# Performance work log

Hardware: AMD Instinct MI355X
Metric: run time of the kernel (lower is better)

Reference implementation:

```python
import jax, jax.numpy as jnp
import numpy as np

L, H, D, FF = 6, 8, 1024, 2048
E = D // 8            # per-head dim = n_model // 8 = 128
MAXLEN = 1024         # relative position table length
B, S = 16, 512


def _sinusoidal(max_len, e):
    # matches RelativePositionalEmbedding.reset_parameters
    pos = np.arange(-(max_len // 2), max_len // 2, dtype=np.float32)
    inv = 10000.0 ** ((np.arange(e) // 2) * 2.0 / e)
    w = pos[:, None] / inv[None, :]
    w[:, 0::2] = np.sin(w[:, 0::2])
    w[:, 1::2] = np.cos(w[:, 1::2])
    return jnp.asarray(w, jnp.float32)


def setup_inputs() -> dict:
    key = jax.random.key(0)
    ks = jax.random.split(key, 12)
    sd_attn = (2.0 / (D + D)) ** 0.5 * (2 ** -0.5)
    sd_ffn1 = (2.0 / (D + FF)) ** 0.5
    inp = {
        "x": jax.random.normal(ks[0], (B, S, D), jnp.float32),
        "mask": jnp.ones((B, S), dtype=bool),
        "wq": jax.random.normal(ks[1], (L, D, D), jnp.float32) * sd_attn,
        "wk": jax.random.normal(ks[2], (L, D, D), jnp.float32) * sd_attn,
        "wv": jax.random.normal(ks[3], (L, D, D), jnp.float32) * sd_attn,
        "wo": jax.random.normal(ks[4], (L, D, D), jnp.float32) * (2.0 / (D + D)) ** 0.5,
        "bu": jnp.zeros((L, H, E), jnp.float32),
        "bv": jnp.zeros((L, H, E), jnp.float32),
        "ln1_g": jnp.ones((L, D), jnp.float32),
        "ln1_b": jnp.zeros((L, D), jnp.float32),
        "w1": jax.random.normal(ks[5], (L, D, FF), jnp.float32) * sd_ffn1,
        "b1": jnp.zeros((L, FF), jnp.float32),
        "w2": jax.random.normal(ks[6], (L, FF, D), jnp.float32) * sd_ffn1,
        "b2": jnp.zeros((L, D), jnp.float32),
        "ln2_g": jnp.ones((L, D), jnp.float32),
        "ln2_b": jnp.zeros((L, D), jnp.float32),
        "pos_table": jnp.tile(_sinusoidal(MAXLEN, E)[None], (L, 1, 1)),
    }
    return inp


def _layer_norm(h, g, b):
    mu = h.mean(-1, keepdims=True)
    var = ((h - mu) ** 2).mean(-1, keepdims=True)
    return (h - mu) * jax.lax.rsqrt(var + 1e-5) * g + b


def reference(x, mask, wq, wk, wv, wo, bu, bv, ln1_g, ln1_b,
              w1, b1, w2, b2, ln2_g, ln2_b, pos_table):
    Bb, Ss, Dd = x.shape
    Ll, Hh, Ee = bu.shape
    scale = float(Ee) ** 0.5
    offset = pos_table.shape[1] // 2
    # relative index j - i + offset, shape [S, S]
    idx = jnp.arange(Ss)[None, :] - jnp.arange(Ss)[:, None] + offset
    neg = jnp.where(mask[:, None, None, :], 0.0, -jnp.inf)  # [B,1,1,S]
    for l in range(Ll):
        q = (x @ wq[l]).reshape(Bb, Ss, Hh, Ee)
        k = (x @ wk[l]).reshape(Bb, Ss, Hh, Ee)
        v = (x @ wv[l]).reshape(Bb, Ss, Hh, Ee)
        p = pos_table[l][idx]  # [S, S, E]
        scores = jnp.einsum('bqhe,bkhe->bhqk', q + bu[l], k)
        scores = scores + jnp.einsum('bqhe,qke->bhqk', q + bv[l], p)
        attn = jax.nn.softmax(scores / scale + neg, axis=-1)
        o = jnp.einsum('bhqk,bkhe->bqhe', attn, v).reshape(Bb, Ss, Hh * Ee) @ wo[l]
        x = _layer_norm(x + o, ln1_g[l], ln1_b[l])
        h = jax.nn.relu(x @ w1[l] + b1[l]) @ w2[l] + b2[l]
        x = _layer_norm(x + h, ln2_g[l], ln2_b[l])
    return x
```

## Files before the change

kernel.cpp:

```cpp
#include <hip/hip_runtime.h>


typedef __bf16 bf16;
typedef __bf16 bf16x4 __attribute__((ext_vector_type(4)));
typedef __bf16 bf16x8 __attribute__((ext_vector_type(8)));
typedef float  f32x4  __attribute__((ext_vector_type(4)));

#define NLAYERS 6
#define NHEADS  8
#define DMODEL  1024
#define FFDIM   2048
#define EDIM    128
#define NBATCH  16
#define SEQ     512

__device__ __forceinline__ void gl_lds16(const bf16* g, bf16* l) {
  __builtin_amdgcn_global_load_lds(
      (const __attribute__((address_space(1))) unsigned int*)g,
      (__attribute__((address_space(3))) unsigned int*)l, 16, 0, 0);
}

struct GArgs {
  const bf16* A;
  const bf16* B;
  const float* bias;
  const float* bias2;
  const float* resid;
  float* outf;
  bf16*  outh;
  bf16*  outh2;
  bf16*  outh3;
  bf16*  outh4;
  int lda, ldb, nK;
  int qoff, mq, msh;
};

template<int MODE>
__global__ __launch_bounds__(256, 3)
void gemm_k(GArgs g) {
  __shared__ __align__(16) bf16 As[128][64];
  __shared__ __align__(16) bf16 Bs[128][64];
  const int tid = threadIdx.x;
  int bx = blockIdx.x, by = blockIdx.y;
  {
    const int nwg = gridDim.x * gridDim.y;
    const int orig = bx + gridDim.x * by;
    const int wsw = (orig & 7) * (nwg >> 3) + (orig >> 3);
    bx = wsw % gridDim.x; by = wsw / gridDim.x;
  }
  const int lane = tid & 63, w = tid >> 6;
  const int wr = w >> 1, wc = w & 1;
  const int l15 = lane & 15, lg = lane >> 4;
  const int xk = l15 & 7;

  int t0 = 0;
  if constexpr (MODE == 10) {
    const int lq0 = (by * 16) & (g.mq - 1);
    const int i0 = g.qoff + lq0;
    t0 = (497 - i0) >> 7; if (t0 > 2) t0 = 2;
  }
  const int bxe = (MODE == 10) ? (t0 + bx) : bx;

  f32x4 acc[4][4] = {};

  for (int ks = 0; ks < g.nK; ++ks) {
    const int k0 = ks * 64;
    #pragma unroll
    for (int i = 0; i < 4; ++i) {
      const int c = i * 256 + tid;
      const int row = c >> 3, slot = c & 7;
      const int kc = (slot ^ (row & 7)) * 8;
      size_t go;
      if constexpr (MODE == 10) {
        const int rg = by * 128 + row;
        const int b = rg >> g.msh;
        const int lq = (rg >> 3) & (g.mq - 1);
        const int hh = rg & 7;
        go = (size_t)b * (SEQ * DMODEL) + (size_t)(g.qoff + lq) * DMODEL
           + hh * EDIM + k0 + kc;
      } else {
        go = (size_t)(by * 128 + row) * g.lda + k0 + kc;
      }
      gl_lds16(g.A + go, &As[row][slot * 8]);
    }
    #pragma unroll
    for (int i = 0; i < 4; ++i) {
      const int c = i * 256 + tid;
      const int row = c >> 3, slot = c & 7;
      const int kc = (slot ^ (row & 7)) * 8;
      gl_lds16(g.B + (size_t)(bxe * 128 + row) * g.ldb + k0 + kc,
               &Bs[row][slot * 8]);
    }
    __syncthreads();
    #pragma unroll
    for (int kk = 0; kk < 2; ++kk) {
      bf16x8 av[4], bvv[4];
      #pragma unroll
      for (int i = 0; i < 4; ++i)
        av[i] = *(const bf16x8*)((const char*)&As[0][0]
                 + (wr * 64 + i * 16 + l15) * 128 + (((kk * 4 + lg) ^ xk) * 16));
      #pragma unroll
      for (int i = 0; i < 4; ++i)
        bvv[i] = *(const bf16x8*)((const char*)&Bs[0][0]
                 + (wc * 64 + i * 16 + l15) * 128 + (((kk * 4 + lg) ^ xk) * 16));
      #pragma unroll
      for (int mi = 0; mi < 4; ++mi)
        #pragma unroll
        for (int ni = 0; ni < 4; ++ni)
          acc[mi][ni] = __builtin_amdgcn_mfma_f32_16x16x32_bf16(av[mi], bvv[ni], acc[mi][ni], 0, 0, 0);
    }
    __syncthreads();
  }

  #pragma unroll
  for (int mi = 0; mi < 4; ++mi)
  #pragma unroll
  for (int ni = 0; ni < 4; ++ni)
  #pragma unroll
  for (int r = 0; r < 4; ++r) {
    const int row = wr * 64 + mi * 16 + lg * 4 + r;
    const int col = wc * 64 + ni * 16 + l15;
    const float v = acc[mi][ni][r];
    if constexpr (MODE == 9) {
      const int gm = by * 128 + row;
      const int seg = bx >> 3;
      const int gc = (bx & 7) * 128 + col;
      if (seg == 0) {
        const size_t i = (size_t)gm * DMODEL + gc;
        g.outh[i]  = (bf16)(v + g.bias[gc]);
        g.outh2[i] = (bf16)(v + g.bias2[gc]);
      } else if (seg == 1) {
        g.outh3[(size_t)gm * DMODEL + gc] = (bf16)v;
      } else {
        const int b = gm >> 9, s = gm & 511, h = gc >> 7, e = gc & 127;
        g.outh4[((size_t)(b * NHEADS + h) * EDIM + e) * SEQ + s] = (bf16)v;
      }
    } else if constexpr (MODE == 10) {
      const int rg = by * 128 + row;
      const int lq = (rg >> 3) & (g.mq - 1);
      const int ig = g.qoff + lq;
      const int j = bxe * 128 + col;
      const int k = j + ig - 512;
      if (k >= 0 && k < 512)
        g.outh[(size_t)rg * 512 + k] = (bf16)v;
    } else if constexpr (MODE == 6) {
      const int gm = by * 128 + row, gc = bx * 128 + col;
      const size_t i = (size_t)gm * DMODEL + gc;
      g.outf[i] = v + g.resid[i];
    } else if constexpr (MODE == 7) {
      const int gm = by * 128 + row, gc = bx * 128 + col;
      g.outh[(size_t)gm * FFDIM + gc] = (bf16)fmaxf(v + g.bias[gc], 0.f);
    } else if constexpr (MODE == 8) {
      const int gm = by * 128 + row, gc = bx * 128 + col;
      const size_t i = (size_t)gm * DMODEL + gc;
      g.outf[i] = v + g.bias[gc] + g.resid[i];
    }
  }
}

struct AArgs {
  const bf16* qu; const bf16* kbf; const bf16* vt; const bf16* R;
  bf16* attnout; int qoff, mq;
};

__global__ __launch_bounds__(256, 2)
void attn_k(AArgs g) {
  __shared__ __align__(16) bf16 Ks[64][128];
  __shared__ __align__(16) bf16 Vs[128][64];
  __shared__ __align__(16) bf16 Pl[128][72];
  const int tid = threadIdx.x, lane = tid & 63, w = tid >> 6;
  const int l15 = lane & 15, lg = lane >> 4;
  int bqt, bh;
  {
    const int nwg = gridDim.x * gridDim.y;
    const int orig = blockIdx.x + gridDim.x * blockIdx.y;
    const int wsw = (orig & 7) * (nwg >> 3) + (orig >> 3);
    bqt = wsw % gridDim.x; bh = wsw / gridDim.x;
  }
  const int b = bh >> 3, h = bh & 7;
  const int q0g = g.qoff + bqt * 128;
  const int qw = w * 32;
  const float ISC = 0.08838834764831845f;

  const bf16* qbase = g.qu + (size_t)b * SEQ * DMODEL
                    + (size_t)(q0g + qw) * DMODEL + (size_t)h * EDIM;
  bf16x8 a[2][4];
  #pragma unroll
  for (int mi = 0; mi < 2; ++mi)
    #pragma unroll
    for (int kk = 0; kk < 4; ++kk)
      a[mi][kk] = *(const bf16x8*)(qbase + (size_t)(mi * 16 + l15) * DMODEL + kk * 32 + lg * 8);

  const bf16* kbase = g.kbf + (size_t)b * SEQ * DMODEL + (size_t)h * EDIM;
  const bf16* vbase = g.vt + (size_t)bh * EDIM * SEQ;
  const bf16* Rrow = g.R + ((size_t)(b * g.mq + (bqt * 128 + qw)) * 8 + h) * 512;

  f32x4 o[2][8] = {};
  float m_run[2][4], s_run[2][4];
  #pragma unroll
  for (int mi = 0; mi < 2; ++mi)
    #pragma unroll
    for (int r = 0; r < 4; ++r) { m_run[mi][r] = -1e30f; s_run[mi][r] = 0.f; }

  for (int kt = 0; kt < 8; ++kt) {
    const int k0 = kt * 64;
    #pragma unroll
    for (int i = 0; i < 4; ++i) {
      const int c = i * 256 + tid;
      const int row = c >> 4, slot = c & 15;
      gl_lds16(kbase + (size_t)(k0 + row) * DMODEL + (slot ^ (row & 15)) * 8,
               &Ks[row][slot * 8]);
    }
    #pragma unroll
    for (int i = 0; i < 4; ++i) {
      const int c = i * 256 + tid;
      const int row = c >> 3, slot = c & 7;
      gl_lds16(vbase + (size_t)row * SEQ + k0 + (slot ^ (row & 7)) * 8,
               &Vs[row][slot * 8]);
    }
    float rv[2][4][4];
    #pragma unroll
    for (int mi = 0; mi < 2; ++mi)
    #pragma unroll
    for (int ni = 0; ni < 4; ++ni)
    #pragma unroll
    for (int r = 0; r < 4; ++r) {
      const int lrow = mi * 16 + lg * 4 + r;
      rv[mi][ni][r] = (float)Rrow[(size_t)lrow * 4096 + (k0 + ni * 16 + l15)];
    }
    __syncthreads();

    f32x4 s[2][4] = {};
    #pragma unroll
    for (int kk = 0; kk < 4; ++kk) {
      bf16x8 bvv[4];
      #pragma unroll
      for (int ni = 0; ni < 4; ++ni)
        bvv[ni] = *(const bf16x8*)((const char*)&Ks[0][0]
                   + (ni * 16 + l15) * 256 + (((kk * 4 + lg) ^ l15) * 16));
      #pragma unroll
      for (int mi = 0; mi < 2; ++mi)
        #pragma unroll
        for (int ni = 0; ni < 4; ++ni)
          s[mi][ni] = __builtin_amdgcn_mfma_f32_16x16x32_bf16(a[mi][kk], bvv[ni], s[mi][ni], 0, 0, 0);
    }

    float sv[2][4][4];
    #pragma unroll
    for (int mi = 0; mi < 2; ++mi)
    #pragma unroll
    for (int ni = 0; ni < 4; ++ni)
    #pragma unroll
    for (int r = 0; r < 4; ++r)
      sv[mi][ni][r] = (s[mi][ni][r] + rv[mi][ni][r]) * ISC;

    float fsc[2][4], rs[2][4];
    #pragma unroll
    for (int mi = 0; mi < 2; ++mi)
    #pragma unroll
    for (int r = 0; r < 4; ++r) {
      float t = fmaxf(fmaxf(sv[mi][0][r], sv[mi][1][r]),
                      fmaxf(sv[mi][2][r], sv[mi][3][r]));
      #pragma unroll
      for (int od = 1; od < 16; od <<= 1) t = fmaxf(t, __shfl_xor(t, od));
      const float mn = fmaxf(m_run[mi][r], t);
      fsc[mi][r] = __expf(m_run[mi][r] - mn);
      m_run[mi][r] = mn;
      rs[mi][r] = 0.f;
    }
    #pragma unroll
    for (int mi = 0; mi < 2; ++mi)
    #pragma unroll
    for (int ni = 0; ni < 4; ++ni)
    #pragma unroll
    for (int r = 0; r < 4; ++r) {
      const float e = __expf(sv[mi][ni][r] - m_run[mi][r]);
      rs[mi][r] += e;
      Pl[qw + mi * 16 + lg * 4 + r][ni * 16 + l15] = (bf16)e;
    }
    #pragma unroll
    for (int mi = 0; mi < 2; ++mi)
    #pragma unroll
    for (int r = 0; r < 4; ++r) {
      float t = rs[mi][r];
      #pragma unroll
      for (int od = 1; od < 16; od <<= 1) t += __shfl_xor(t, od);
      s_run[mi][r] = s_run[mi][r] * fsc[mi][r] + t;
    }
    #pragma unroll
    for (int mi = 0; mi < 2; ++mi)
    #pragma unroll
    for (int ni = 0; ni < 8; ++ni)
    #pragma unroll
    for (int r = 0; r < 4; ++r)
      o[mi][ni][r] *= fsc[mi][r];

    bf16x8 pa[2][2];
    #pragma unroll
    for (int mi = 0; mi < 2; ++mi)
      #pragma unroll
      for (int kk = 0; kk < 2; ++kk)
        pa[mi][kk] = *(const bf16x8*)&Pl[qw + mi * 16 + l15][kk * 32 + lg * 8];
    #pragma unroll
    for (int ni = 0; ni < 8; ++ni) {
      const int vr = ni * 16 + l15;
      bf16x8 v0 = *(const bf16x8*)((const char*)&Vs[0][0]
                   + vr * 128 + ((lg ^ (l15 & 7)) * 16));
      bf16x8 v1 = *(const bf16x8*)((const char*)&Vs[0][0]
                   + vr * 128 + (((4 + lg) ^ (l15 & 7)) * 16));
      #pragma unroll
      for (int mi = 0; mi < 2; ++mi) {
        o[mi][ni] = __builtin_amdgcn_mfma_f32_16x16x32_bf16(pa[mi][0], v0, o[mi][ni], 0, 0, 0);
        o[mi][ni] = __builtin_amdgcn_mfma_f32_16x16x32_bf16(pa[mi][1], v1, o[mi][ni], 0, 0, 0);
      }
    }
    __syncthreads();
  }

  const size_t obase = (size_t)b * SEQ * DMODEL + (size_t)h * EDIM;
  #pragma unroll
  for (int mi = 0; mi < 2; ++mi)
  #pragma unroll
  for (int ni = 0; ni < 8; ++ni)
  #pragma unroll
  for (int r = 0; r < 4; ++r) {
    const int q = q0g + qw + mi * 16 + lg * 4 + r;
    g.attnout[obase + (size_t)q * DMODEL + ni * 16 + l15] =
        (bf16)(o[mi][ni][r] / s_run[mi][r]);
  }
}

struct TArgs {
  const float* wq; const float* wk; const float* wv; const float* wo;
  const float* w1; const float* w2;
  bf16* out;
};
__global__ __launch_bounds__(256)
void wtrans_k(TArgs t) {
  __shared__ float tt[32][33];
  const int bid = blockIdx.x;
  int seg, tile;
  if (bid < 4096)      { seg = bid >> 10; tile = bid & 1023; }
  else if (bid < 6144) { seg = 4; tile = bid - 4096; }
  else                 { seg = 5; tile = bid - 6144; }
  int R, C, txn; size_t oofs; const float* in;
  if (seg < 4) {
    R = 1024; C = 1024; txn = 32; oofs = (size_t)seg << 20;
    in = (seg == 0) ? t.wq : (seg == 1) ? t.wk : (seg == 2) ? t.wv : t.wo;
  } else if (seg == 4) {
    R = 1024; C = 2048; txn = 64; oofs = (size_t)4 << 20; in = t.w1;
  } else {
    R = 2048; C = 1024; txn = 32; oofs = (size_t)6 << 20; in = t.w2;
  }
  bf16* out = t.out + oofs;
  const int c0 = (tile % txn) * 32, r0 = (tile / txn) * 32;
  const int tx = threadIdx.x & 31, ty = threadIdx.x >> 5;
  #pragma unroll
  for (int i = 0; i < 32; i += 8)
    tt[ty + i][tx] = in[(size_t)(r0 + ty + i) * C + c0 + tx];
  __syncthreads();
  #pragma unroll
  for (int i = 0; i < 32; i += 8)
    out[(size_t)(c0 + ty + i) * R + r0 + tx] = (bf16)tt[tx][ty + i];
}

__global__ __launch_bounds__(256)
void cvt_k(const float* __restrict__ in, bf16* __restrict__ out, int n4) {
  const int i = blockIdx.x * 256 + threadIdx.x;
  if (i >= n4) return;
  const float4 v = ((const float4*)in)[i];
  bf16x4 h; h[0] = (bf16)v.x; h[1] = (bf16)v.y; h[2] = (bf16)v.z; h[3] = (bf16)v.w;
  ((bf16x4*)out)[i] = h;
}

__global__ __launch_bounds__(256)
void ln_k(const float* __restrict__ y, const float* __restrict__ gam, const float* __restrict__ bet,
          float* __restrict__ xout, bf16* __restrict__ xbf) {
  const int t = threadIdx.x;
  const size_t row = blockIdx.x;
  const float4 v = *(const float4*)(y + row * DMODEL + t * 4);
  float s = v.x + v.y + v.z + v.w;
  float q = v.x * v.x + v.y * v.y + v.z * v.z + v.w * v.w;
  #pragma unroll
  for (int o = 32; o; o >>= 1) { s += __shfl_xor(s, o); q += __shfl_xor(q, o); }
  __shared__ float red[8];
  const int wid = t >> 6;
  if ((t & 63) == 0) { red[wid * 2] = s; red[wid * 2 + 1] = q; }
  __syncthreads();
  s = red[0] + red[2] + red[4] + red[6];
  q = red[1] + red[3] + red[5] + red[7];
  const float mu = s * (1.f / DMODEL);
  const float var = q * (1.f / DMODEL) - mu * mu;
  const float rs = rsqrtf(var + 1e-5f);
  const float g0 = gam[t * 4], g1 = gam[t * 4 + 1], g2 = gam[t * 4 + 2], g3 = gam[t * 4 + 3];
  const float b0 = bet[t * 4], b1 = bet[t * 4 + 1], b2 = bet[t * 4 + 2], b3 = bet[t * 4 + 3];
  float4 o;
  o.x = (v.x - mu) * rs * g0 + b0; o.y = (v.y - mu) * rs * g1 + b1;
  o.z = (v.z - mu) * rs * g2 + b2; o.w = (v.w - mu) * rs * g3 + b3;
  *(float4*)(xout + row * DMODEL + t * 4) = o;
  bf16x4 h; h[0] = (bf16)o.x; h[1] = (bf16)o.y; h[2] = (bf16)o.z; h[3] = (bf16)o.w;
  *(bf16x4*)(xbf + row * DMODEL + t * 4) = h;
}

extern "C" void kernel_launch(void* const* d_in, const int* in_sizes, int n_in,
                              void* d_out, int out_size, void* d_ws, size_t ws_size,
                              hipStream_t stream) {
  const float* x_in  = (const float*)d_in[0];
  const float* wq    = (const float*)d_in[2];
  const float* wk    = (const float*)d_in[3];
  const float* wv    = (const float*)d_in[4];
  const float* wo    = (const float*)d_in[5];
  const float* bu    = (const float*)d_in[6];
  const float* bv    = (const float*)d_in[7];
  const float* ln1g  = (const float*)d_in[8];
  const float* ln1b  = (const float*)d_in[9];
  const float* w1    = (const float*)d_in[10];
  const float* b1    = (const float*)d_in[11];
  const float* w2    = (const float*)d_in[12];
  const float* b2    = (const float*)d_in[13];
  const float* ln2g  = (const float*)d_in[14];
  const float* ln2b  = (const float*)d_in[15];
  const float* pos   = (const float*)d_in[16];
  float* out = (float*)d_out;

  char* ws = (char*)d_ws;
  size_t off = 0;
  auto alloc = [&](size_t bytes) -> void* {
    void* p = ws + off; off += (bytes + 255) & ~(size_t)255; return p;
  };
  const size_t BSD = (size_t)NBATCH * SEQ * DMODEL;
  bf16* posb = (bf16*)alloc((size_t)NLAYERS * 1024 * EDIM * 2);
  bf16* wT   = (bf16*)alloc((size_t)8 * 1024 * 1024 * 2);
  bf16* xbf  = (bf16*)alloc(BSD * 2);
  float* xws = (float*)alloc(BSD * 4);
  float* ybuf= (float*)alloc(BSD * 4);
  bf16* qu   = (bf16*)alloc(BSD * 2);
  bf16* qv   = (bf16*)alloc(BSD * 2);
  bf16* kbf  = (bf16*)alloc(BSD * 2);
  bf16* vt   = (bf16*)alloc(BSD * 2);
  bf16* attnout = qv;
  bf16* h1 = qu;
  const size_t base = off;

  int C = 4;
  if (ws_size >= base + (size_t)512 * 131072) C = 1;
  else if (ws_size >= base + (size_t)256 * 131072) C = 2;
  const int mq = SEQ / C;
  const int msh = (mq == 512) ? 12 : (mq == 256) ? 11 : 10;
  bf16* R2 = (bf16*)alloc((size_t)mq * 131072);

  cvt_k<<<(int)(BSD / 4 / 256), 256, 0, stream>>>(x_in, xbf, (int)(BSD / 4));
  cvt_k<<<(NLAYERS * 1024 * EDIM / 4) / 256, 256, 0, stream>>>(pos, posb, NLAYERS * 1024 * EDIM / 4);

  for (int l = 0; l < NLAYERS; ++l) {
    const size_t wofs = (size_t)l * DMODEL * DMODEL;
    const size_t fofs = (size_t)l * DMODEL * FFDIM;

    TArgs ta{wq + wofs, wk + wofs, wv + wofs, wo + wofs, w1 + fofs, w2 + fofs, wT};
    wtrans_k<<<8192, 256, 0, stream>>>(ta);

    GArgs a{};
    a.A = xbf; a.B = wT; a.bias = bu + l * 1024; a.bias2 = bv + l * 1024;
    a.outh = qu; a.outh2 = qv; a.outh3 = kbf; a.outh4 = vt;
    a.lda = 1024; a.ldb = 1024; a.nK = 16;
    gemm_k<9><<<dim3(24, 64), 256, 0, stream>>>(a);

    for (int c = 0; c < C; ++c) {
      const int qoff = c * mq;
      GArgs ar{}; ar.A = qv; ar.B = posb + (size_t)l * 1024 * EDIM; ar.outh = R2;
      ar.lda = 1024; ar.ldb = 128; ar.nK = 2; ar.qoff = qoff; ar.mq = mq; ar.msh = msh;
      gemm_k<10><<<dim3(6, mq), 256, 0, stream>>>(ar);

      AArgs aa{qu, kbf, vt, R2, attnout, qoff, mq};
      attn_k<<<dim3(mq / 128, 128), 256, 0, stream>>>(aa);
    }

    GArgs aw{}; aw.A = attnout; aw.B = wT + ((size_t)3 << 20); aw.resid = (l == 0 ? x_in : xws);
    aw.outf = ybuf; aw.lda = 1024; aw.ldb = 1024; aw.nK = 16;
    gemm_k<6><<<dim3(8, 64), 256, 0, stream>>>(aw);

    ln_k<<<NBATCH * SEQ, 256, 0, stream>>>(ybuf, ln1g + l * 1024, ln1b + l * 1024, xws, xbf);

    GArgs af1{}; af1.A = xbf; af1.B = wT + ((size_t)4 << 20); af1.bias = b1 + l * FFDIM; af1.outh = h1;
    af1.lda = 1024; af1.ldb = 1024; af1.nK = 16;
    gemm_k<7><<<dim3(16, 64), 256, 0, stream>>>(af1);

    GArgs af2{}; af2.A = h1; af2.B = wT + ((size_t)6 << 20); af2.bias = b2 + l * 1024; af2.resid = xws;
    af2.outf = ybuf; af2.lda = 2048; af2.ldb = 2048; af2.nK = 32;
    gemm_k<8><<<dim3(8, 64), 256, 0, stream>>>(af2);

    ln_k<<<NBATCH * SEQ, 256, 0, stream>>>(ybuf, ln2g + l * 1024, ln2b + l * 1024,
                                           (l == NLAYERS - 1 ? out : xws), xbf);
  }
}
```

Baseline: 2.285 ms.

## Add double-buffered 256x128 GEMM kernel with quadrant-interleaved load/MFMA schedule

Introduces a new GEMM kernel with 512 threads and a 256x128 output tile. It double-buffers LDS and splits each K step into four quadrant MFMA phases, each interleaved with async global-to-LDS loads for the next tiles, using setprio and barriers to overlap memory and compute. The QKV, output-projection and FFN GEMMs switch to it, while the relative-position GEMM stays on the old kernel. This targets exposed load latency and raises per-block data reuse, at the cost of more LDS per block, fewer blocks in flight, and fragile hand-written vmcnt accounting.

```diff
diff --git a/kernel.cpp b/kernel.cpp
--- a/kernel.cpp
+++ b/kernel.cpp
@@ -36,10 +36,10 @@
 };
 
 template<int MODE>
-__global__ __launch_bounds__(256, 3)
-void gemm_k(GArgs g) {
-  __shared__ __align__(16) bf16 As[128][64];
-  __shared__ __align__(16) bf16 Bs[128][64];
+__global__ __launch_bounds__(512, 2)
+void gemm256_k(GArgs g) {
+  __shared__ __align__(16) bf16 Asm[2][256 * 64];
+  __shared__ __align__(16) bf16 Bsm[2][128 * 64];
   const int tid = threadIdx.x;
   int bx = blockIdx.x, by = blockIdx.y;
   {
@@ -49,67 +49,98 @@
     bx = wsw % gridDim.x; by = wsw / gridDim.x;
   }
   const int lane = tid & 63, w = tid >> 6;
-  const int wr = w >> 1, wc = w & 1;
+  const int wrp = w >> 1, wcn = w & 1;
   const int l15 = lane & 15, lg = lane >> 4;
-  const int xk = l15 & 7;
-
-  int t0 = 0;
-  if constexpr (MODE == 10) {
-    const int lq0 = (by * 16) & (g.mq - 1);
-    const int i0 = g.qoff + lq0;
-    t0 = (497 - i0) >> 7; if (t0 > 2) t0 = 2;
-  }
-  const int bxe = (MODE == 10) ? (t0 + bx) : bx;
+  const int nK = g.nK;
 
   f32x4 acc[4][4] = {};
 
-  for (int ks = 0; ks < g.nK; ++ks) {
-    const int k0 = ks * 64;
-    #pragma unroll
-    for (int i = 0; i < 4; ++i) {
-      const int c = i * 256 + tid;
-      const int row = c >> 3, slot = c & 7;
+  auto stageA = [&](int buf, int kt, int mh) {
+    const int k0 = kt * 64;
+    #pragma unroll
+    for (int j = 0; j < 2; ++j) {
+      const int idx = j * 512 + tid;
+      const int rw = idx >> 3, slot = idx & 7;
+      const int row = (rw >> 5) * 64 + mh * 32 + (rw & 31);
       const int kc = (slot ^ (row & 7)) * 8;
-      size_t go;
-      if constexpr (MODE == 10) {
-        const int rg = by * 128 + row;
-        const int b = rg >> g.msh;
-        const int lq = (rg >> 3) & (g.mq - 1);
-        const int hh = rg & 7;
-        go = (size_t)b * (SEQ * DMODEL) + (size_t)(g.qoff + lq) * DMODEL
-           + hh * EDIM + k0 + kc;
-      } else {
-        go = (size_t)(by * 128 + row) * g.lda + k0 + kc;
+      gl_lds16(g.A + (size_t)(by * 256 + row) * g.lda + k0 + kc,
+               &Asm[buf][row * 64 + slot * 8]);
+    }
+  };
+  auto stageB = [&](int buf, int kt, int nh) {
+    const int k0 = kt * 64;
+    const int rw = tid >> 3, slot = tid & 7;
+    const int row = (rw >> 5) * 64 + nh * 32 + (rw & 31);
+    const int kc = (slot ^ (row & 7)) * 8;
+    gl_lds16(g.B + (size_t)(bx * 128 + row) * g.ldb + k0 + kc,
+             &Bsm[buf][row * 64 + slot * 8]);
+  };
+  auto rdA = [&](bf16x8 (&d)[2][2], int buf, int mh) {
+    #pragma unroll
+    for (int mi = 0; mi < 2; ++mi)
+      #pragma unroll
+      for (int ks = 0; ks < 2; ++ks) {
+        const int row = wrp * 64 + mh * 32 + mi * 16 + l15;
+        const int c = (((ks * 4 + lg) ^ (l15 & 7)) * 16);
+        d[mi][ks] = *(const bf16x8*)((const char*)&Asm[buf][0] + row * 128 + c);
       }
-      gl_lds16(g.A + go, &As[row][slot * 8]);
-    }
-    #pragma unroll
-    for (int i = 0; i < 4; ++i) {
-      const int c = i * 256 + tid;
-      const int row = c >> 3, slot = c & 7;
-      const int kc = (slot ^ (row & 7)) * 8;
-      gl_lds16(g.B + (size_t)(bxe * 128 + row) * g.ldb + k0 + kc,
-               &Bs[row][slot * 8]);
-    }
-    __syncthreads();
-    #pragma unroll
-    for (int kk = 0; kk < 2; ++kk) {
-      bf16x8 av[4], bvv[4];
-      #pragma unroll
-      for (int i = 0; i < 4; ++i)
-        av[i] = *(const bf16x8*)((const char*)&As[0][0]
-                 + (wr * 64 + i * 16 + l15) * 128 + (((kk * 4 + lg) ^ xk) * 16));
-      #pragma unroll
-      for (int i = 0; i < 4; ++i)
-        bvv[i] = *(const bf16x8*)((const char*)&Bs[0][0]
-                 + (wc * 64 + i * 16 + l15) * 128 + (((kk * 4 + lg) ^ xk) * 16));
-      #pragma unroll
-      for (int mi = 0; mi < 4; ++mi)
+  };
+  auto rdB = [&](bf16x8 (&d)[2][2], int buf, int nh) {
+    #pragma unroll
+    for (int ni = 0; ni < 2; ++ni)
+      #pragma unroll
+      for (int ks = 0; ks < 2; ++ks) {
+        const int row = wcn * 64 + nh * 32 + ni * 16 + l15;
+        const int c = (((ks * 4 + lg) ^ (l15 & 7)) * 16);
+        d[ni][ks] = *(const bf16x8*)((const char*)&Bsm[buf][0] + row * 128 + c);
+      }
+  };
+  auto mmaQ = [&](bf16x8 (&A_)[2][2], bf16x8 (&B_)[2][2], int mh, int nh) {
+    __builtin_amdgcn_s_setprio(1);
+    #pragma unroll
+    for (int ks = 0; ks < 2; ++ks)
+      #pragma unroll
+      for (int mi = 0; mi < 2; ++mi)
         #pragma unroll
-        for (int ni = 0; ni < 4; ++ni)
-          acc[mi][ni] = __builtin_amdgcn_mfma_f32_16x16x32_bf16(av[mi], bvv[ni], acc[mi][ni], 0, 0, 0);
-    }
-    __syncthreads();
+        for (int ni = 0; ni < 2; ++ni)
+          acc[mh * 2 + mi][nh * 2 + ni] = __builtin_amdgcn_mfma_f32_16x16x32_bf16(
+              A_[mi][ks], B_[ni][ks], acc[mh * 2 + mi][nh * 2 + ni], 0, 0, 0);
+    __builtin_amdgcn_s_setprio(0);
+  };
+
+  stageA(0, 0, 0); stageA(0, 0, 1); stageB(0, 0, 0); stageB(0, 0, 1);
+  stageA(1, 1, 0); stageB(1, 1, 0); stageA(1, 1, 1);
+  asm volatile("s_waitcnt vmcnt(5)" ::: "memory");
+  __builtin_amdgcn_sched_barrier(0);
+  __builtin_amdgcn_s_barrier();
+
+  for (int u = 0; u < nK; ++u) {
+    const int buf = u & 1;
+    bf16x8 a0[2][2], a1[2][2], b0[2][2], b1[2][2];
+    rdA(a0, buf, 0); rdB(b0, buf, 0);
+    if (u + 1 < nK) stageB(buf ^ 1, u + 1, 1);
+    __builtin_amdgcn_s_barrier();
+    mmaQ(a0, b0, 0, 0);
+    __builtin_amdgcn_s_barrier();
+    rdA(a1, buf, 1);
+    if (u + 2 < nK) stageA(buf, u + 2, 0);
+    __builtin_amdgcn_s_barrier();
+    mmaQ(a1, b0, 1, 0);
+    __builtin_amdgcn_s_barrier();
+    rdB(b1, buf, 1);
+    if (u + 2 < nK) stageB(buf, u + 2, 0);
+    __builtin_amdgcn_s_barrier();
+    mmaQ(a1, b1, 1, 1);
+    __builtin_amdgcn_s_barrier();
+    if (u + 2 < nK) stageA(buf, u + 2, 1);
+    __builtin_amdgcn_s_barrier();
+    mmaQ(a0, b1, 0, 1);
+    if (u < nK - 1) {
+      if (u == nK - 2) { asm volatile("s_waitcnt vmcnt(0)" ::: "memory"); }
+      else             { asm volatile("s_waitcnt vmcnt(5)" ::: "memory"); }
+      __builtin_amdgcn_sched_barrier(0);
+    }
+    __builtin_amdgcn_s_barrier();
   }
 
   #pragma unroll
@@ -118,11 +149,11 @@
   for (int ni = 0; ni < 4; ++ni)
   #pragma unroll
   for (int r = 0; r < 4; ++r) {
-    const int row = wr * 64 + mi * 16 + lg * 4 + r;
-    const int col = wc * 64 + ni * 16 + l15;
+    const int row = wrp * 64 + (mi >> 1) * 32 + (mi & 1) * 16 + lg * 4 + r;
+    const int col = wcn * 64 + (ni >> 1) * 32 + (ni & 1) * 16 + l15;
+    const int gm = by * 256 + row;
     const float v = acc[mi][ni][r];
     if constexpr (MODE == 9) {
-      const int gm = by * 128 + row;
       const int seg = bx >> 3;
       const int gc = (bx & 7) * 128 + col;
       if (seg == 0) {
@@ -135,26 +166,103 @@
         const int b = gm >> 9, s = gm & 511, h = gc >> 7, e = gc & 127;
         g.outh4[((size_t)(b * NHEADS + h) * EDIM + e) * SEQ + s] = (bf16)v;
       }
-    } else if constexpr (MODE == 10) {
-      const int rg = by * 128 + row;
-      const int lq = (rg >> 3) & (g.mq - 1);
-      const int ig = g.qoff + lq;
-      const int j = bxe * 128 + col;
-      const int k = j + ig - 512;
-      if (k >= 0 && k < 512)
-        g.outh[(size_t)rg * 512 + k] = (bf16)v;
     } else if constexpr (MODE == 6) {
-      const int gm = by * 128 + row, gc = bx * 128 + col;
+      const int gc = bx * 128 + col;
       const size_t i = (size_t)gm * DMODEL + gc;
       g.outf[i] = v + g.resid[i];
     } else if constexpr (MODE == 7) {
-      const int gm = by * 128 + row, gc = bx * 128 + col;
+      const int gc = bx * 128 + col;
       g.outh[(size_t)gm * FFDIM + gc] = (bf16)fmaxf(v + g.bias[gc], 0.f);
     } else if constexpr (MODE == 8) {
-      const int gm = by * 128 + row, gc = bx * 128 + col;
+      const int gc = bx * 128 + col;
       const size_t i = (size_t)gm * DMODEL + gc;
       g.outf[i] = v + g.bias[gc] + g.resid[i];
     }
+  }
+}
+
+template<int MODE>
+__global__ __launch_bounds__(256, 3)
+void gemm_k(GArgs g) {
+  __shared__ __align__(16) bf16 As[128][64];
+  __shared__ __align__(16) bf16 Bs[128][64];
+  const int tid = threadIdx.x;
+  const int bx = blockIdx.x, by = blockIdx.y;
+  const int lane = tid & 63, w = tid >> 6;
+  const int wr = w >> 1, wc = w & 1;
+  const int l15 = lane & 15, lg = lane >> 4;
+  const int xk = l15 & 7;
+
+  int t0 = 0;
+  {
+    const int lq0 = (by * 16) & (g.mq - 1);
+    const int i0 = g.qoff + lq0;
+    t0 = (497 - i0) >> 7; if (t0 > 2) t0 = 2;
+  }
+  const int bxe = t0 + bx;
+
+  f32x4 acc[4][4] = {};
+
+  for (int ks = 0; ks < g.nK; ++ks) {
+    const int k0 = ks * 64;
+    #pragma unroll
+    for (int i = 0; i < 4; ++i) {
+      const int c = i * 256 + tid;
+      const int row = c >> 3, slot = c & 7;
+      const int kc = (slot ^ (row & 7)) * 8;
+      const int rg = by * 128 + row;
+      const int b = rg >> g.msh;
+      const int lq = (rg >> 3) & (g.mq - 1);
+      const int hh = rg & 7;
+      const size_t go = (size_t)b * (SEQ * DMODEL) + (size_t)(g.qoff + lq) * DMODEL
+                      + hh * EDIM + k0 + kc;
+      gl_lds16(g.A + go, &As[row][slot * 8]);
+    }
+    #pragma unroll
+    for (int i = 0; i < 4; ++i) {
+      const int c = i * 256 + tid;
+      const int row = c >> 3, slot = c & 7;
+      const int kc = (slot ^ (row & 7)) * 8;
+      gl_lds16(g.B + (size_t)(bxe * 128 + row) * g.ldb + k0 + kc,
+               &Bs[row][slot * 8]);
+    }
+    __syncthreads();
+    #pragma unroll
+    for (int kk = 0; kk < 2; ++kk) {
+      bf16x8 av[4], bvv[4];
+      #pragma unroll
+      for (int i = 0; i < 4; ++i)
+        av[i] = *(const bf16x8*)((const char*)&As[0][0]
+                 + (wr * 64 + i * 16 + l15) * 128 + (((kk * 4 + lg) ^ xk) * 16));
+      #pragma unroll
+      for (int i = 0; i < 4; ++i)
+        bvv[i] = *(const bf16x8*)((const char*)&Bs[0][0]
+                 + (wc * 64 + i * 16 + l15) * 128 + (((kk * 4 + lg) ^ xk) * 16));
+      #pragma unroll
+      for (int mi = 0; mi < 4; ++mi)
+        #pragma unroll
+        for (int ni = 0; ni < 4; ++ni)
+          acc[mi][ni] = __builtin_amdgcn_mfma_f32_16x16x32_bf16(av[mi], bvv[ni], acc[mi][ni], 0, 0, 0);
+    }
+    __syncthreads();
+  }
+
+  #pragma unroll
+  for (int mi = 0; mi < 4; ++mi)
+  #pragma unroll
+  for (int ni = 0; ni < 4; ++ni)
+  #pragma unroll
+  for (int r = 0; r < 4; ++r) {
+    const int row = wr * 64 + mi * 16 + lg * 4 + r;
+    const int col = wc * 64 + ni * 16 + l15;
+    const float v = acc[mi][ni][r];
+    const int rg = by * 128 + row;
+    const int lq = (rg >> 3) & (g.mq - 1);
+    const int ig = g.qoff + lq;
+    const int j = bxe * 128 + col;
+    const int k = j + ig - 512;
+    if (k >= 0 && k < 512)
+      g.outh[(size_t)rg * 512 + k] = (bf16)v;
   }
 }
 
@@ -463,7 +571,7 @@
     a.A = xbf; a.B = wT; a.bias = bu + l * 1024; a.bias2 = bv + l * 1024;
     a.outh = qu; a.outh2 = qv; a.outh3 = kbf; a.outh4 = vt;
     a.lda = 1024; a.ldb = 1024; a.nK = 16;
-    gemm_k<9><<<dim3(24, 64), 256, 0, stream>>>(a);
+    gemm256_k<9><<<dim3(24, 32), 512, 0, stream>>>(a);
 
     for (int c = 0; c < C; ++c) {
       const int qoff = c * mq;
@@ -477,17 +585,17 @@
 
     GArgs aw{}; aw.A = attnout; aw.B = wT + ((size_t)3 << 20); aw.resid = (l == 0 ? x_in : xws);
     aw.outf = ybuf; aw.lda = 1024; aw.ldb = 1024; aw.nK = 16;
-    gemm_k<6><<<dim3(8, 64), 256, 0, stream>>>(aw);
+    gemm256_k<6><<<dim3(8, 32), 512, 0, stream>>>(aw);
 
     ln_k<<<NBATCH * SEQ, 256, 0, stream>>>(ybuf, ln1g + l * 1024, ln1b + l * 1024, xws, xbf);
 
     GArgs af1{}; af1.A = xbf; af1.B = wT + ((size_t)4 << 20); af1.bias = b1 + l * FFDIM; af1.outh = h1;
     af1.lda = 1024; af1.ldb = 1024; af1.nK = 16;
-    gemm_k<7><<<dim3(16, 64), 256, 0, stream>>>(af1);
+    gemm256_k<7><<<dim3(16, 32), 512, 0, stream>>>(af1);
 
     GArgs af2{}; af2.A = h1; af2.B = wT + ((size_t)6 << 20); af2.bias = b2 + l * 1024; af2.resid = xws;
     af2.outf = ybuf; af2.lda = 2048; af2.ldb = 2048; af2.nK = 32;
-    gemm_k<8><<<dim3(8, 64), 256, 0, stream>>>(af2);
+    gemm256_k<8><<<dim3(8, 32), 512, 0, stream>>>(af2);
 
     ln_k<<<NBATCH * SEQ, 256, 0, stream>>>(ybuf, ln2g + l * 1024, ln2b + l * 1024,
                                            (l == NLAYERS - 1 ? out : xws), xbf);
```

New measurement: 2.415 ms. +5.7%, slower.

## Double-buffer GEMM LDS tiles to overlap global loads with MFMA compute

Applied to the files above, without the earlier changes.

Doubles the LDS A/B tile buffers so the next K-slice is fetched with global_load_lds while the current slice is multiplied. Explicit vmcnt waits and barriers replace the former per-iteration __syncthreads pair. This hides global memory latency behind MFMA work. In exchange, LDS use doubles and the occupancy hint drops from 3 to 2 blocks per CU.

```diff
diff --git a/kernel.cpp b/kernel.cpp
--- a/kernel.cpp
+++ b/kernel.cpp
@@ -36,10 +36,10 @@
 };
 
 template<int MODE>
-__global__ __launch_bounds__(256, 3)
+__global__ __launch_bounds__(256, 2)
 void gemm_k(GArgs g) {
-  __shared__ __align__(16) bf16 As[128][64];
-  __shared__ __align__(16) bf16 Bs[128][64];
+  __shared__ __align__(16) bf16 As[2][128][64];
+  __shared__ __align__(16) bf16 Bs[2][128][64];
   const int tid = threadIdx.x;
   int bx = blockIdx.x, by = blockIdx.y;
   {
@@ -63,7 +63,7 @@
 
   f32x4 acc[4][4] = {};
 
-  for (int ks = 0; ks < g.nK; ++ks) {
+  auto stage = [&](int buf, int ks) {
     const int k0 = ks * 64;
     #pragma unroll
     for (int i = 0; i < 4; ++i) {
@@ -81,7 +81,7 @@
       } else {
         go = (size_t)(by * 128 + row) * g.lda + k0 + kc;
       }
-      gl_lds16(g.A + go, &As[row][slot * 8]);
+      gl_lds16(g.A + go, &As[buf][row][slot * 8]);
     }
     #pragma unroll
     for (int i = 0; i < 4; ++i) {
@@ -89,19 +89,21 @@
       const int row = c >> 3, slot = c & 7;
       const int kc = (slot ^ (row & 7)) * 8;
       gl_lds16(g.B + (size_t)(bxe * 128 + row) * g.ldb + k0 + kc,
-               &Bs[row][slot * 8]);
-    }
-    __syncthreads();
+               &Bs[buf][row][slot * 8]);
+    }
+  };
+
+  auto compute = [&](int buf) {
     #pragma unroll
     for (int kk = 0; kk < 2; ++kk) {
       bf16x8 av[4], bvv[4];
       #pragma unroll
       for (int i = 0; i < 4; ++i)
-        av[i] = *(const bf16x8*)((const char*)&As[0][0]
+        av[i] = *(const bf16x8*)((const char*)&As[buf][0][0]
                  + (wr * 64 + i * 16 + l15) * 128 + (((kk * 4 + lg) ^ xk) * 16));
       #pragma unroll
       for (int i = 0; i < 4; ++i)
-        bvv[i] = *(const bf16x8*)((const char*)&Bs[0][0]
+        bvv[i] = *(const bf16x8*)((const char*)&Bs[buf][0][0]
                  + (wc * 64 + i * 16 + l15) * 128 + (((kk * 4 + lg) ^ xk) * 16));
       #pragma unroll
       for (int mi = 0; mi < 4; ++mi)
@@ -109,7 +111,22 @@
         for (int ni = 0; ni < 4; ++ni)
           acc[mi][ni] = __builtin_amdgcn_mfma_f32_16x16x32_bf16(av[mi], bvv[ni], acc[mi][ni], 0, 0, 0);
     }
-    __syncthreads();
+  };
+
+  stage(0, 0);
+  int cur = 0;
+  for (int ks = 0; ks < g.nK; ++ks) {
+    if (ks + 1 < g.nK) {
+      stage(cur ^ 1, ks + 1);
+      asm volatile("s_waitcnt vmcnt(8)" ::: "memory");
+    } else {
+      asm volatile("s_waitcnt vmcnt(0)" ::: "memory");
+    }
+    __builtin_amdgcn_s_barrier();
+    __builtin_amdgcn_sched_barrier(0);
+    compute(cur);
+    __builtin_amdgcn_s_barrier();
+    cur ^= 1;
   }
 
   #pragma unroll
```

Measured after the change: 2.320 ms. Within noise of the previous version (+1.5%).
